# Kernel optimization log

Measured on AMD Instinct MI355X. Metric: run time of the kernel, lower is better.

## Reference

```python
import jax, jax.numpy as jnp
import numpy as np

B, S, D, H, L, E, FF = 16, 1024, 384, 8, 3, 8, 768
DH = D // H
TOP_K = 2


def _ln(x, s, b):
    m = x.mean(-1, keepdims=True)
    v = x.var(-1, keepdims=True)
    return (x - m) * jax.lax.rsqrt(v + 1e-5) * s + b


def setup_inputs() -> dict:
    key = jax.random.key(0)
    ks = jax.random.split(key, 12)
    def n(k, shp, scale=0.02):
        return jax.random.normal(k, shp, jnp.float32) * scale
    return dict(
        x=jax.random.normal(ks[0], (B, S, 1), jnp.float32),
        proj_w=n(ks[1], (1, D)), proj_b=jnp.zeros((D,), jnp.float32),
        qkv_w=n(ks[2], (L, D, 3 * D)), qkv_b=jnp.zeros((L, 3 * D), jnp.float32),
        out_w=n(ks[3], (L, D, D)), out_b=jnp.zeros((L, D), jnp.float32),
        n1_s=jnp.ones((L, D), jnp.float32), n1_b=jnp.zeros((L, D), jnp.float32),
        n2_s=jnp.ones((L, D), jnp.float32), n2_b=jnp.zeros((L, D), jnp.float32),
        gate_w=n(ks[4], (L, D, E)),
        e_w1=n(ks[5], (L, E, D, FF)), e_b1=jnp.zeros((L, E, FF), jnp.float32),
        e_w2=n(ks[6], (L, E, FF, D)), e_b2=jnp.zeros((L, E, D), jnp.float32),
        att_w=n(ks[7], (D,)), att_b=jnp.zeros((), jnp.float32),
        head_w=n(ks[8], (D, 1)), head_b=jnp.zeros((1,), jnp.float32),
    )


def reference(x, proj_w, proj_b, qkv_w, qkv_b, out_w, out_b,
              n1_s, n1_b, n2_s, n2_b, gate_w, e_w1, e_b1, e_w2, e_b2,
              att_w, att_b, head_w, head_b):
    # feature projection: [B,S,1] -> [B,S,D]
    h = x @ proj_w + proj_b
    total_moe = jnp.zeros((), h.dtype)
    scale = np.float32(1.0 / np.sqrt(DH))
    for l in range(L):
        # --- pre-norm multi-head self-attention ---
        xn = _ln(h, n1_s[l], n1_b[l])
        qkv = xn @ qkv_w[l] + qkv_b[l]
        q, k, v = jnp.split(qkv, 3, axis=-1)
        q = q.reshape(B, S, H, DH)
        k = k.reshape(B, S, H, DH)
        v = v.reshape(B, S, H, DH)
        attn = jax.nn.softmax(jnp.einsum('bqhd,bkhd->bhqk', q, k) * scale, axis=-1)
        ao = jnp.einsum('bhqk,bkhd->bqhd', attn, v).reshape(B, S, D)
        h = h + (ao @ out_w[l] + out_b[l])
        # --- pre-norm top-2 gated MoE FFN ---
        xn2 = _ln(h, n2_s[l], n2_b[l])
        probs = jax.nn.softmax(xn2 @ gate_w[l], axis=-1)            # [B,S,E]
        topv, topi = jax.lax.top_k(probs, TOP_K)
        gates = topv / topv.sum(-1, keepdims=True)                  # renormalized top-2
        full = (jax.nn.one_hot(topi, E, dtype=h.dtype) * gates[..., None]).sum(-2)  # [B,S,E]
        moe_out = jnp.zeros_like(h)
        for e in range(E):  # fixed small expert loop
            ye = jax.nn.relu(xn2 @ e_w1[l, e] + e_b1[l, e]) @ e_w2[l, e] + e_b2[l, e]
            moe_out = moe_out + full[..., e:e + 1] * ye
        h = h + moe_out
        # switch-style load-balancing aux loss
        importance = probs.reshape(-1, E).mean(0)
        load = (full > 0).astype(h.dtype).reshape(-1, E).mean(0)
        total_moe = total_moe + E * jnp.sum(importance * load)
    w = jax.nn.softmax(h @ att_w + att_b, axis=1)                   # [B,S]
    pooled = jnp.einsum('bs,bsd->bd', w, h)
    rul = pooled @ head_w + head_b                                  # [B,1]
    return rul, total_moe
```

## Files before the change

kernel.cpp:

```cpp
#include <hip/hip_runtime.h>
#include <hip/hip_bf16.h>
#include <math.h>

#define TOKENS 16384
#define DMODEL 384
#define SEQ 1024
#define NHEAD 8
#define DHEAD 48
#define NEXP 8
#define FFDIM 768
#define NL 3

typedef __bf16 bf16x8 __attribute__((ext_vector_type(8)));
typedef __bf16 bf16x4 __attribute__((ext_vector_type(4)));
typedef float f32x4 __attribute__((ext_vector_type(4)));

__global__ void init_kernel(float* total_moe) { *total_moe = 0.f; }

__global__ void zero_cnt_kernel(int* counts, float* sum_probs) {
  int t = threadIdx.x;
  if (t < NEXP) { counts[t] = 0; sum_probs[t] = 0.f; }
}

__global__ void finalize_kernel(const float* total_moe, float* out) { out[16] = *total_moe; }

__global__ __launch_bounds__(256) void proj_kernel(const float* __restrict__ x,
    const float* __restrict__ pw, const float* __restrict__ pb, float* __restrict__ h) {
  int i = blockIdx.x * 256 + threadIdx.x;
  int t = i / DMODEL;
  int d = i - t * DMODEL;
  h[i] = x[t] * pw[d] + pb[d];
}

__global__ __launch_bounds__(256) void convw_kernel(const float* __restrict__ src,
    __bf16* __restrict__ dst, int K, int N) {
  __shared__ float t[32][33];
  size_t boff = (size_t)blockIdx.z * K * N;
  src += boff; dst += boff;
  int k0 = blockIdx.y * 32, n0 = blockIdx.x * 32;
  int tx = threadIdx.x & 31, ty = threadIdx.x >> 5;
#pragma unroll
  for (int i = 0; i < 32; i += 8) t[ty + i][tx] = src[(size_t)(k0 + ty + i) * N + n0 + tx];
  __syncthreads();
#pragma unroll
  for (int i = 0; i < 32; i += 8)
    dst[(size_t)(n0 + ty + i) * K + k0 + tx] = (__bf16)t[tx][ty + i];
}

__global__ __launch_bounds__(384) void ln_kernel(const float* __restrict__ src,
    __bf16* __restrict__ dst, const float* __restrict__ gs, const float* __restrict__ gb) {
  int row = blockIdx.x, tid = threadIdx.x;
  float v = src[(size_t)row * DMODEL + tid];
  float sum = v, sq = v * v;
#pragma unroll
  for (int off = 32; off; off >>= 1) { sum += __shfl_xor(sum, off); sq += __shfl_xor(sq, off); }
  __shared__ float rs[6], rq[6];
  __shared__ float smean, sinv;
  int wid = tid >> 6;
  if ((tid & 63) == 0) { rs[wid] = sum; rq[wid] = sq; }
  __syncthreads();
  if (tid == 0) {
    float S = 0.f, Q = 0.f;
    for (int w = 0; w < 6; w++) { S += rs[w]; Q += rq[w]; }
    float mean = S / (float)DMODEL;
    float var = Q / (float)DMODEL - mean * mean;
    smean = mean; sinv = rsqrtf(var + 1e-5f);
  }
  __syncthreads();
  dst[(size_t)row * DMODEL + tid] = (__bf16)((v - smean) * sinv * gs[tid] + gb[tid]);
}

template<int MODE>
__global__ __launch_bounds__(256) void mgemm_kernel(
    const __bf16* __restrict__ Abf, const __bf16* __restrict__ Wt,
    const float* __restrict__ bias, float* __restrict__ Cf, __bf16* __restrict__ Cb,
    __bf16* __restrict__ pQ, __bf16* __restrict__ pK, __bf16* __restrict__ pV,
    const int* __restrict__ counts, const int* __restrict__ offs,
    const int* __restrict__ tok_list, const float* __restrict__ gate_list,
    int N, int K) {
  int e = 0, cnt = 0, base = 0;
  const int* tl = nullptr;
  int m0 = blockIdx.y * 128;
  int n0 = blockIdx.x * 128;
  if constexpr (MODE == 2 || MODE == 3) {
    e = blockIdx.z;
    cnt = counts[e];
    if (m0 >= cnt) return;
    base = offs[e];
    tl = tok_list + e * TOKENS;
    Wt += (size_t)e * N * K;
    bias += (size_t)e * N;
  }
  __shared__ __align__(16) __bf16 As[2][128][72];
  __shared__ __align__(16) __bf16 Bs[2][128][72];
  int tid = threadIdx.x;
  int w = tid >> 6, lane = tid & 63, c = lane & 15, g = lane >> 4;
  int arow[4], acol[4], brow[4], bcol4[4];
  long tok[4];
#pragma unroll
  for (int i = 0; i < 4; i++) {
    int chunk = tid + 256 * i;
    arow[i] = chunk >> 3;
    acol[i] = (chunk & 7) * 8;
    brow[i] = chunk >> 3;
    bcol4[i] = (chunk & 7) * 8;
    int mr = m0 + arow[i];
    if constexpr (MODE == 2)      tok[i] = (mr < cnt) ? (long)(tl[mr] & 0xFFFF) : -1;
    else if constexpr (MODE == 3) tok[i] = (mr < cnt) ? (long)(base + mr) : -1;
    else                          tok[i] = mr;
  }
  f32x4 acc[2][8];
#pragma unroll
  for (int m = 0; m < 2; m++)
#pragma unroll
    for (int n = 0; n < 8; n++) { acc[m][n][0] = 0.f; acc[m][n][1] = 0.f; acc[m][n][2] = 0.f; acc[m][n][3] = 0.f; }

  bf16x8 ra[4], rb[4];
  int nk = K >> 6;
#pragma unroll
  for (int i = 0; i < 4; i++) {
    bf16x8 v = {};
    if (tok[i] >= 0) v = *(const bf16x8*)&Abf[(size_t)tok[i] * K + acol[i]];
    ra[i] = v;
    rb[i] = *(const bf16x8*)&Wt[(size_t)(n0 + brow[i]) * K + bcol4[i]];
  }
  for (int kt = 0; kt < nk; kt++) {
    int cb = kt & 1;
#pragma unroll
    for (int i = 0; i < 4; i++) {
      *(bf16x8*)&As[cb][arow[i]][acol[i]] = ra[i];
      *(bf16x8*)&Bs[cb][brow[i]][bcol4[i]] = rb[i];
    }
    __syncthreads();
    if (kt + 1 < nk) {
      int k0 = (kt + 1) << 6;
#pragma unroll
      for (int i = 0; i < 4; i++) {
        bf16x8 v = {};
        if (tok[i] >= 0) v = *(const bf16x8*)&Abf[(size_t)tok[i] * K + k0 + acol[i]];
        ra[i] = v;
        rb[i] = *(const bf16x8*)&Wt[(size_t)(n0 + brow[i]) * K + k0 + bcol4[i]];
      }
    }
#pragma unroll
    for (int kk = 0; kk < 2; kk++) {
      bf16x8 a0 = *(const bf16x8*)&As[cb][w * 32 + c][kk * 32 + g * 8];
      bf16x8 a1 = *(const bf16x8*)&As[cb][w * 32 + 16 + c][kk * 32 + g * 8];
#pragma unroll
      for (int n = 0; n < 8; n++) {
        bf16x8 b = *(const bf16x8*)&Bs[cb][n * 16 + c][kk * 32 + g * 8];
        acc[0][n] = __builtin_amdgcn_mfma_f32_16x16x32_bf16(a0, b, acc[0][n], 0, 0, 0);
        acc[1][n] = __builtin_amdgcn_mfma_f32_16x16x32_bf16(a1, b, acc[1][n], 0, 0, 0);
      }
    }
  }
#pragma unroll
  for (int m = 0; m < 2; m++) {
    int row = w * 32 + m * 16 + 4 * g;
#pragma unroll
    for (int n = 0; n < 8; n++) {
      int col = n0 + n * 16 + c;
      float bv = bias[col];
#pragma unroll
      for (int r = 0; r < 4; r++) {
        float v = acc[m][n][r] + bv;
        int lr = row + r;
        if constexpr (MODE == 0) {
          int t = m0 + lr;
          int b = t >> 10, s = t & 1023;
          int which = col / 384;
          int rem = col - which * 384;
          int hd = rem / 48;
          int d = rem - hd * 48;
          size_t bh = (size_t)(b * 8 + hd);
          if (which == 0)      pQ[(bh * 1024 + s) * 48 + d] = (__bf16)(v * 0.14433756729740643f);
          else if (which == 1) pK[(bh * 1024 + s) * 48 + d] = (__bf16)v;
          else                 pV[(bh * 48 + d) * 1024 + s] = (__bf16)v;
        } else if constexpr (MODE == 1) {
          Cf[(size_t)(m0 + lr) * N + col] += v;
        } else if constexpr (MODE == 2) {
          if (m0 + lr < cnt) Cb[(size_t)(base + m0 + lr) * N + col] = (__bf16)fmaxf(v, 0.f);
        } else {
          if (m0 + lr < cnt) {
            int entry = tl[m0 + lr];
            int t = entry & 0xFFFF, a = entry >> 16;
            float gv = gate_list[e * TOKENS + m0 + lr];
            Cb[((size_t)a * TOKENS + t) * DMODEL + col] = (__bf16)(gv * v);
          }
        }
      }
    }
  }
}

__global__ __launch_bounds__(256) void combine_kernel(float* __restrict__ h,
    const __bf16* __restrict__ ab) {
  size_t i = ((size_t)blockIdx.x * 256 + threadIdx.x) * 8;
  bf16x8 a0 = *(const bf16x8*)&ab[i];
  bf16x8 a1 = *(const bf16x8*)&ab[(size_t)TOKENS * DMODEL + i];
  float* hp = h + i;
#pragma unroll
  for (int j = 0; j < 8; j++) hp[j] += (float)a0[j] + (float)a1[j];
}

__global__ __launch_bounds__(256) void attn_kernel(const __bf16* __restrict__ Qh,
    const __bf16* __restrict__ Kh, const __bf16* __restrict__ VTh,
    __bf16* __restrict__ ao) {
  __shared__ __align__(16) __bf16 Ks[64][56];
  __shared__ __align__(16) __bf16 Vt[48][72];
  __shared__ __align__(16) __bf16 Ps[4][16][72];
  int bh = blockIdx.x;
  int q0 = blockIdx.y * 64;
  int tid = threadIdx.x;
  int w = tid >> 6, lane = tid & 63, c = lane & 15, g = lane >> 4;

  const __bf16* qrow = Qh + ((size_t)bh * 1024 + q0 + w * 16 + c) * 48;
  bf16x8 qb0 = *(const bf16x8*)&qrow[g * 8];
  bf16x8 qb1 = {};
  if (g < 2) qb1 = *(const bf16x8*)&qrow[32 + g * 8];

  const __bf16* kb = Kh + (size_t)bh * 1024 * 48;
  const __bf16* vb = VTh + (size_t)bh * 48 * 1024;

  int r0 = tid / 6, p0 = tid - r0 * 6;
  __bf16* dst0 = &Ks[r0][p0 * 8];
  int off0 = r0 * 48 + p0 * 8;
  int e1 = tid + 256;
  __bf16* dst1; int off1; bool v1;
  if (e1 < 384) { int r = e1 / 6, p = e1 - r * 6; dst1 = &Ks[r][p * 8]; off1 = r * 48 + p * 8; v1 = false; }
  else          { int i = e1 - 384; int d = i >> 3, p = i & 7; dst1 = &Vt[d][p * 8]; off1 = d * 1024 + p * 8; v1 = true; }
  int i2 = tid + 512 - 384;
  int d2 = i2 >> 3, p2 = i2 & 7;
  __bf16* dst2 = &Vt[d2][p2 * 8];
  int off2 = d2 * 1024 + p2 * 8;

  f32x4 acc[3];
#pragma unroll
  for (int t = 0; t < 3; t++) { acc[t][0] = 0.f; acc[t][1] = 0.f; acc[t][2] = 0.f; acc[t][3] = 0.f; }
  float lsum = 0.f;

  for (int kt = 0; kt < 16; kt++) {
    __syncthreads();
    const __bf16* kbt = kb + (size_t)kt * 3072;
    const __bf16* vbt = vb + kt * 64;
    *(bf16x8*)dst0 = *(const bf16x8*)(kbt + off0);
    *(bf16x8*)dst1 = *(const bf16x8*)((v1 ? vbt : kbt) + off1);
    *(bf16x8*)dst2 = *(const bf16x8*)(vbt + off2);
    __syncthreads();

    f32x4 s4[4];
#pragma unroll
    for (int f = 0; f < 4; f++) {
      bf16x8 ka0 = *(const bf16x8*)&Ks[f * 16 + c][g * 8];
      bf16x8 ka1 = {};
      if (g < 2) ka1 = *(const bf16x8*)&Ks[f * 16 + c][32 + g * 8];
      f32x4 z = {};
      z = __builtin_amdgcn_mfma_f32_16x16x32_bf16(ka0, qb0, z, 0, 0, 0);
      s4[f] = __builtin_amdgcn_mfma_f32_16x16x32_bf16(ka1, qb1, z, 0, 0, 0);
    }
#pragma unroll
    for (int f = 0; f < 4; f++) {
      float pv0 = __expf(s4[f][0]);
      float pv1 = __expf(s4[f][1]);
      float pv2 = __expf(s4[f][2]);
      float pv3 = __expf(s4[f][3]);
      lsum += (pv0 + pv1) + (pv2 + pv3);
      bf16x4 pk = { (__bf16)pv0, (__bf16)pv1, (__bf16)pv2, (__bf16)pv3 };
      *(bf16x4*)&Ps[w][c][f * 16 + 4 * g] = pk;
    }
    bf16x8 pa0 = *(const bf16x8*)&Ps[w][c][g * 8];
    bf16x8 pa1 = *(const bf16x8*)&Ps[w][c][32 + g * 8];
#pragma unroll
    for (int t = 0; t < 3; t++) {
      bf16x8 vb0 = *(const bf16x8*)&Vt[t * 16 + c][g * 8];
      bf16x8 vb1 = *(const bf16x8*)&Vt[t * 16 + c][32 + g * 8];
      acc[t] = __builtin_amdgcn_mfma_f32_16x16x32_bf16(pa0, vb0, acc[t], 0, 0, 0);
      acc[t] = __builtin_amdgcn_mfma_f32_16x16x32_bf16(pa1, vb1, acc[t], 0, 0, 0);
    }
  }
  float lt = lsum;
  lt += __shfl_xor(lt, 16, 64);
  lt += __shfl_xor(lt, 32, 64);
  float linv[4];
#pragma unroll
  for (int r = 0; r < 4; r++) linv[r] = 1.f / __shfl(lt, 4 * g + r, 64);
  int b = bh >> 3, hh = bh & 7;
#pragma unroll
  for (int t = 0; t < 3; t++)
#pragma unroll
    for (int r = 0; r < 4; r++)
      ao[((size_t)(b * SEQ + q0 + w * 16 + 4 * g + r)) * DMODEL + hh * 48 + t * 16 + c] =
          (__bf16)(acc[t][r] * linv[r]);
}

__global__ __launch_bounds__(256) void gate_kernel(const __bf16* __restrict__ xnb,
    const float* __restrict__ gw, int* __restrict__ counts, float* __restrict__ sum_probs,
    int* __restrict__ tok_list, float* __restrict__ gate_list) {
  __shared__ float Gs[NEXP][DMODEL];
  __shared__ float simp[NEXP];
  __shared__ int hist[NEXP], basep[NEXP];
  __shared__ unsigned char tokE[32][2];
  __shared__ float tokG[32][2];
  __shared__ short rankS[32][2];
  int tid = threadIdx.x;
  for (int i = tid; i < DMODEL * NEXP; i += 256) {
    int d = i >> 3, e2 = i & 7;
    Gs[e2][d] = gw[i];
  }
  if (tid < NEXP) { simp[tid] = 0.f; hist[tid] = 0; }
  __syncthreads();
  int w = tid >> 6, lane = tid & 63;
  int tbase = blockIdx.x * 32 + w * 8;
  float impacc[NEXP] = {};
  for (int tt = 0; tt < 8; tt++) {
    int t = tbase + tt;
    float p[NEXP] = {};
#pragma unroll
    for (int j = 0; j < 6; j++) {
      int d = lane + 64 * j;
      float xv = (float)xnb[(size_t)t * DMODEL + d];
#pragma unroll
      for (int e2 = 0; e2 < NEXP; e2++) p[e2] += xv * Gs[e2][d];
    }
#pragma unroll
    for (int off = 32; off; off >>= 1)
#pragma unroll
      for (int e2 = 0; e2 < NEXP; e2++) p[e2] += __shfl_xor(p[e2], off);
    float mx = p[0];
#pragma unroll
    for (int e2 = 1; e2 < NEXP; e2++) mx = fmaxf(mx, p[e2]);
    float s = 0.f;
#pragma unroll
    for (int e2 = 0; e2 < NEXP; e2++) { p[e2] = __expf(p[e2] - mx); s += p[e2]; }
    float inv = 1.f / s;
#pragma unroll
    for (int e2 = 0; e2 < NEXP; e2++) { p[e2] *= inv; impacc[e2] += p[e2]; }
    int i0 = 0; float v0 = p[0];
#pragma unroll
    for (int e2 = 1; e2 < NEXP; e2++) if (p[e2] > v0) { v0 = p[e2]; i0 = e2; }
    int i1 = -1; float v1 = -INFINITY;
#pragma unroll
    for (int e2 = 0; e2 < NEXP; e2++) if (e2 != i0 && p[e2] > v1) { v1 = p[e2]; i1 = e2; }
    if (lane == 0) {
      float gsum = v0 + v1;
      int r0 = atomicAdd(&hist[i0], 1);
      int r1 = atomicAdd(&hist[i1], 1);
      int sl = w * 8 + tt;
      tokE[sl][0] = (unsigned char)i0; tokE[sl][1] = (unsigned char)i1;
      tokG[sl][0] = v0 / gsum;         tokG[sl][1] = v1 / gsum;
      rankS[sl][0] = (short)r0;        rankS[sl][1] = (short)r1;
    }
  }
  if (lane == 0)
#pragma unroll
    for (int e2 = 0; e2 < NEXP; e2++) atomicAdd(&simp[e2], impacc[e2]);
  __syncthreads();
  if (tid < NEXP) {
    basep[tid] = atomicAdd(&counts[tid], hist[tid]);
    atomicAdd(&sum_probs[tid], simp[tid]);
  }
  __syncthreads();
  int t0 = blockIdx.x * 32;
  if (tid < 64) {
    int sl = tid >> 1, a = tid & 1;
    int e2 = tokE[sl][a];
    int pos = basep[e2] + rankS[sl][a];
    tok_list[e2 * TOKENS + pos] = (t0 + sl) | (a << 16);
    gate_list[e2 * TOKENS + pos] = tokG[sl][a];
  }
}

__global__ void aux_kernel(const int* __restrict__ counts, int* __restrict__ offs,
                           const float* __restrict__ sum_probs, float* __restrict__ total_moe) {
  int off = 0;
  float tm = 0.f;
  for (int e = 0; e < NEXP; e++) {
    offs[e] = off;
    off += ((counts[e] + 63) >> 6) << 6;
    tm += sum_probs[e] * (float)counts[e];
  }
  offs[NEXP] = off;
  *total_moe += (float)NEXP * tm / ((float)TOKENS * (float)TOKENS);
}

__global__ __launch_bounds__(256) void head1_kernel(const float* __restrict__ h,
    const float* __restrict__ att_w, const float* __restrict__ att_b,
    float* __restrict__ logits) {
  int tid = threadIdx.x;
  int w = tid >> 6, lane = tid & 63;
  float4 aw0 = *(const float4*)&att_w[lane * 4];
  float2 aw1 = *(const float2*)&att_w[256 + lane * 2];
  float ab = att_b[0];
  for (int i = w; i < 32; i += 4) {
    int t = blockIdx.x * 32 + i;
    const float* hr = h + (size_t)t * DMODEL;
    float4 v4 = *(const float4*)&hr[lane * 4];
    float2 v2 = *(const float2*)&hr[256 + lane * 2];
    float dot = v4.x * aw0.x + v4.y * aw0.y + v4.z * aw0.z + v4.w * aw0.w
              + v2.x * aw1.x + v2.y * aw1.y;
#pragma unroll
    for (int off = 32; off; off >>= 1) dot += __shfl_xor(dot, off);
    if (lane == 0) logits[t] = dot + ab;
  }
}

__global__ __launch_bounds__(256) void head2_kernel(float* __restrict__ logits) {
  int b = blockIdx.x, tid = threadIdx.x;
  int w = tid >> 6, lane = tid & 63;
  float* lb = logits + b * SEQ;
  __shared__ float red[4];
  float lv[4];
  float mx = -INFINITY;
#pragma unroll
  for (int i = 0; i < 4; i++) { lv[i] = lb[tid + 256 * i]; mx = fmaxf(mx, lv[i]); }
#pragma unroll
  for (int off = 32; off; off >>= 1) mx = fmaxf(mx, __shfl_xor(mx, off));
  if (lane == 0) red[w] = mx;
  __syncthreads();
  mx = fmaxf(fmaxf(red[0], red[1]), fmaxf(red[2], red[3]));
  __syncthreads();
  float s = 0.f;
#pragma unroll
  for (int i = 0; i < 4; i++) { lv[i] = __expf(lv[i] - mx); s += lv[i]; }
#pragma unroll
  for (int off = 32; off; off >>= 1) s += __shfl_xor(s, off);
  if (lane == 0) red[w] = s;
  __syncthreads();
  float inv = 1.f / (red[0] + red[1] + red[2] + red[3]);
#pragma unroll
  for (int i = 0; i < 4; i++) lb[tid + 256 * i] = lv[i] * inv;
}

__global__ __launch_bounds__(256) void head3a_kernel(const float* __restrict__ h,
    const float* __restrict__ wnorm, float* __restrict__ partial) {
  int b = blockIdx.x, dc = blockIdx.y, sc = blockIdx.z;
  int tid = threadIdx.x;
  int d = tid & 63, sg = tid >> 6;
  const float* hb = h + (size_t)b * SEQ * DMODEL + dc * 64 + d;
  const float* wb = wnorm + b * SEQ + sc * 64;
  float acc = 0.f;
  int s0 = sc * 64 + sg * 16;
#pragma unroll
  for (int i = 0; i < 16; i++)
    acc += wb[sg * 16 + i] * hb[(size_t)(s0 + i) * DMODEL];
  __shared__ float red[256];
  red[tid] = acc;
  __syncthreads();
  if (sg == 0)
    partial[(((size_t)b * 6 + dc) * 16 + sc) * 64 + d] =
        red[d] + red[64 + d] + red[128 + d] + red[192 + d];
}

__global__ void head3b_kernel(const float* __restrict__ partial,
    const float* __restrict__ head_w, float* __restrict__ part) {
  int b = blockIdx.x, dc = blockIdx.y;
  int d = threadIdx.x;
  const float* pp = partial + (((size_t)b * 6 + dc) * 16) * 64 + d;
  float pooled = 0.f;
#pragma unroll
  for (int sc = 0; sc < 16; sc++) pooled += pp[sc * 64];
  float pd = pooled * head_w[dc * 64 + d];
#pragma unroll
  for (int off = 32; off; off >>= 1) pd += __shfl_xor(pd, off);
  if (d == 0) part[b * 6 + dc] = pd;
}

__global__ void head4_kernel(const float* __restrict__ part,
                             const float* __restrict__ head_b, float* __restrict__ out) {
  int b = threadIdx.x;
  if (b < 16) {
    float s = head_b[0];
#pragma unroll
    for (int dc = 0; dc < 6; dc++) s += part[b * 6 + dc];
    out[b] = s;
  }
}

extern "C" void kernel_launch(void* const* d_in, const int* in_sizes, int n_in,
                              void* d_out, int out_size, void* d_ws, size_t ws_size,
                              hipStream_t stream) {
  (void)in_sizes; (void)n_in; (void)out_size; (void)ws_size;
  const float* x      = (const float*)d_in[0];
  const float* proj_w = (const float*)d_in[1];
  const float* proj_b = (const float*)d_in[2];
  const float* qkv_w  = (const float*)d_in[3];
  const float* qkv_b  = (const float*)d_in[4];
  const float* out_w  = (const float*)d_in[5];
  const float* out_b  = (const float*)d_in[6];
  const float* n1_s   = (const float*)d_in[7];
  const float* n1_b   = (const float*)d_in[8];
  const float* n2_s   = (const float*)d_in[9];
  const float* n2_b   = (const float*)d_in[10];
  const float* gate_w = (const float*)d_in[11];
  const float* e_w1   = (const float*)d_in[12];
  const float* e_b1   = (const float*)d_in[13];
  const float* e_w2   = (const float*)d_in[14];
  const float* e_b2   = (const float*)d_in[15];
  const float* att_w  = (const float*)d_in[16];
  const float* att_b  = (const float*)d_in[17];
  const float* head_w = (const float*)d_in[18];
  const float* head_b = (const float*)d_in[19];
  float* out = (float*)d_out;

  char* wsb = (char*)d_ws;
  float*  h    = (float*)(wsb);
  __bf16* xnb  = (__bf16*)(wsb + 25165824);
  __bf16* aob  = (__bf16*)(wsb + 37748736);
  __bf16* ab   = (__bf16*)(wsb + 25165824);
  __bf16* uni  = (__bf16*)(wsb + 50331648);
  __bf16* Qh   = uni;
  __bf16* Khd  = (__bf16*)(wsb + 62914560);
  __bf16* VTh  = (__bf16*)(wsb + 75497472);
  __bf16* qkvWt = (__bf16*)(wsb + 101449728);
  __bf16* outWt = (__bf16*)(wsb + 104103936);
  __bf16* e1Wt  = (__bf16*)(wsb + 104988672);
  __bf16* e2Wt  = (__bf16*)(wsb + 119144448);
  char* sm = wsb + 133300224;
  int*   counts    = (int*)(sm);
  int*   offs      = (int*)(sm + 64);
  float* sum_probs = (float*)(sm + 128);
  float* total_moe = (float*)(sm + 192);
  int*   tok_list  = (int*)(sm + 256);
  float* gate_list = (float*)(sm + 256 + 524288);
  float* logits    = (float*)(sm + 1048832);
  float* part      = (float*)(sm + 1048832 + 65536);
  float* partial   = (float*)(sm + 1048832 + 131072);

  convw_kernel<<<dim3(36, 12, 3), 256, 0, stream>>>(qkv_w, qkvWt, 384, 1152);
  convw_kernel<<<dim3(12, 12, 3), 256, 0, stream>>>(out_w, outWt, 384, 384);
  convw_kernel<<<dim3(24, 12, 24), 256, 0, stream>>>(e_w1, e1Wt, 384, 768);
  convw_kernel<<<dim3(12, 24, 24), 256, 0, stream>>>(e_w2, e2Wt, 768, 384);

  init_kernel<<<1, 1, 0, stream>>>(total_moe);
  proj_kernel<<<TOKENS * DMODEL / 256, 256, 0, stream>>>(x, proj_w, proj_b, h);

  for (int l = 0; l < NL; l++) {
    ln_kernel<<<TOKENS, 384, 0, stream>>>(h, xnb, n1_s + l * DMODEL, n1_b + l * DMODEL);
    mgemm_kernel<0><<<dim3(9, 128), 256, 0, stream>>>(
        xnb, qkvWt + (size_t)l * 1152 * 384, qkv_b + l * 1152, nullptr, nullptr,
        Qh, Khd, VTh, nullptr, nullptr, nullptr, nullptr, 1152, 384);
    attn_kernel<<<dim3(128, 16), 256, 0, stream>>>(Qh, Khd, VTh, aob);
    mgemm_kernel<1><<<dim3(3, 128), 256, 0, stream>>>(
        aob, outWt + (size_t)l * 384 * 384, out_b + l * 384, h, nullptr,
        nullptr, nullptr, nullptr, nullptr, nullptr, nullptr, nullptr, 384, 384);
    ln_kernel<<<TOKENS, 384, 0, stream>>>(h, xnb, n2_s + l * DMODEL, n2_b + l * DMODEL);
    zero_cnt_kernel<<<1, 64, 0, stream>>>(counts, sum_probs);
    gate_kernel<<<512, 256, 0, stream>>>(xnb, gate_w + (size_t)l * DMODEL * NEXP,
                                         counts, sum_probs, tok_list, gate_list);
    aux_kernel<<<1, 1, 0, stream>>>(counts, offs, sum_probs, total_moe);
    mgemm_kernel<2><<<dim3(6, 128, 8), 256, 0, stream>>>(
        xnb, e1Wt + (size_t)l * 8 * 768 * 384, e_b1 + l * 8 * FFDIM, nullptr, uni,
        nullptr, nullptr, nullptr, counts, offs, tok_list, nullptr, 768, 384);
    mgemm_kernel<3><<<dim3(3, 128, 8), 256, 0, stream>>>(
        uni, e2Wt + (size_t)l * 8 * 384 * 768, e_b2 + l * 8 * DMODEL, nullptr, ab,
        nullptr, nullptr, nullptr, counts, offs, tok_list, gate_list, 384, 768);
    combine_kernel<<<TOKENS * DMODEL / (256 * 8), 256, 0, stream>>>(h, ab);
  }

  head1_kernel<<<512, 256, 0, stream>>>(h, att_w, att_b, logits);
  head2_kernel<<<16, 256, 0, stream>>>(logits);
  head3a_kernel<<<dim3(16, 6, 16), 256, 0, stream>>>(h, logits, partial);
  head3b_kernel<<<dim3(16, 6), 64, 0, stream>>>(partial, head_w, part);
  head4_kernel<<<1, 64, 0, stream>>>(part, head_b, out);
  finalize_kernel<<<1, 1, 0, stream>>>(total_moe, out);
}
```

Before: 1.073 ms.

## Fuse MoE expert up and down projections into one kernel per token tile

```diff
diff --git a/kernel.cpp b/kernel.cpp
--- a/kernel.cpp
+++ b/kernel.cpp
@@ -73,41 +73,21 @@
 template<int MODE>
 __global__ __launch_bounds__(256) void mgemm_kernel(
     const __bf16* __restrict__ Abf, const __bf16* __restrict__ Wt,
-    const float* __restrict__ bias, float* __restrict__ Cf, __bf16* __restrict__ Cb,
+    const float* __restrict__ bias, float* __restrict__ Cf,
     __bf16* __restrict__ pQ, __bf16* __restrict__ pK, __bf16* __restrict__ pV,
-    const int* __restrict__ counts, const int* __restrict__ offs,
-    const int* __restrict__ tok_list, const float* __restrict__ gate_list,
     int N, int K) {
-  int e = 0, cnt = 0, base = 0;
-  const int* tl = nullptr;
   int m0 = blockIdx.y * 128;
   int n0 = blockIdx.x * 128;
-  if constexpr (MODE == 2 || MODE == 3) {
-    e = blockIdx.z;
-    cnt = counts[e];
-    if (m0 >= cnt) return;
-    base = offs[e];
-    tl = tok_list + e * TOKENS;
-    Wt += (size_t)e * N * K;
-    bias += (size_t)e * N;
-  }
   __shared__ __align__(16) __bf16 As[2][128][72];
   __shared__ __align__(16) __bf16 Bs[2][128][72];
   int tid = threadIdx.x;
   int w = tid >> 6, lane = tid & 63, c = lane & 15, g = lane >> 4;
-  int arow[4], acol[4], brow[4], bcol4[4];
-  long tok[4];
+  int arow[4], acol[4];
 #pragma unroll
   for (int i = 0; i < 4; i++) {
     int chunk = tid + 256 * i;
     arow[i] = chunk >> 3;
     acol[i] = (chunk & 7) * 8;
-    brow[i] = chunk >> 3;
-    bcol4[i] = (chunk & 7) * 8;
-    int mr = m0 + arow[i];
-    if constexpr (MODE == 2)      tok[i] = (mr < cnt) ? (long)(tl[mr] & 0xFFFF) : -1;
-    else if constexpr (MODE == 3) tok[i] = (mr < cnt) ? (long)(base + mr) : -1;
-    else                          tok[i] = mr;
   }
   f32x4 acc[2][8];
 #pragma unroll
@@ -119,27 +99,23 @@
   int nk = K >> 6;
 #pragma unroll
   for (int i = 0; i < 4; i++) {
-    bf16x8 v = {};
-    if (tok[i] >= 0) v = *(const bf16x8*)&Abf[(size_t)tok[i] * K + acol[i]];
-    ra[i] = v;
-    rb[i] = *(const bf16x8*)&Wt[(size_t)(n0 + brow[i]) * K + bcol4[i]];
+    ra[i] = *(const bf16x8*)&Abf[(size_t)(m0 + arow[i]) * K + acol[i]];
+    rb[i] = *(const bf16x8*)&Wt[(size_t)(n0 + arow[i]) * K + acol[i]];
   }
   for (int kt = 0; kt < nk; kt++) {
     int cb = kt & 1;
 #pragma unroll
     for (int i = 0; i < 4; i++) {
       *(bf16x8*)&As[cb][arow[i]][acol[i]] = ra[i];
-      *(bf16x8*)&Bs[cb][brow[i]][bcol4[i]] = rb[i];
+      *(bf16x8*)&Bs[cb][arow[i]][acol[i]] = rb[i];
     }
     __syncthreads();
     if (kt + 1 < nk) {
       int k0 = (kt + 1) << 6;
 #pragma unroll
       for (int i = 0; i < 4; i++) {
-        bf16x8 v = {};
-        if (tok[i] >= 0) v = *(const bf16x8*)&Abf[(size_t)tok[i] * K + k0 + acol[i]];
-        ra[i] = v;
-        rb[i] = *(const bf16x8*)&Wt[(size_t)(n0 + brow[i]) * K + k0 + bcol4[i]];
+        ra[i] = *(const bf16x8*)&Abf[(size_t)(m0 + arow[i]) * K + k0 + acol[i]];
+        rb[i] = *(const bf16x8*)&Wt[(size_t)(n0 + arow[i]) * K + k0 + acol[i]];
       }
     }
 #pragma unroll
@@ -176,21 +152,114 @@
           if (which == 0)      pQ[(bh * 1024 + s) * 48 + d] = (__bf16)(v * 0.14433756729740643f);
           else if (which == 1) pK[(bh * 1024 + s) * 48 + d] = (__bf16)v;
           else                 pV[(bh * 48 + d) * 1024 + s] = (__bf16)v;
-        } else if constexpr (MODE == 1) {
+        } else {
           Cf[(size_t)(m0 + lr) * N + col] += v;
-        } else if constexpr (MODE == 2) {
-          if (m0 + lr < cnt) Cb[(size_t)(base + m0 + lr) * N + col] = (__bf16)fmaxf(v, 0.f);
-        } else {
-          if (m0 + lr < cnt) {
-            int entry = tl[m0 + lr];
-            int t = entry & 0xFFFF, a = entry >> 16;
-            float gv = gate_list[e * TOKENS + m0 + lr];
-            Cb[((size_t)a * TOKENS + t) * DMODEL + col] = (__bf16)(gv * v);
-          }
         }
       }
     }
   }
+}
+
+__global__ __launch_bounds__(256) void moe_fused_kernel(
+    const __bf16* __restrict__ xnb, const __bf16* __restrict__ W1t,
+    const __bf16* __restrict__ W2t, const float* __restrict__ b1,
+    const float* __restrict__ b2, __bf16* __restrict__ ab,
+    const int* __restrict__ counts, const int* __restrict__ tok_list,
+    const float* __restrict__ gate_list) {
+  int e = blockIdx.y;
+  int cnt = counts[e];
+  int m0 = blockIdx.x * 32;
+  if (m0 >= cnt) return;
+  const int* tl = tok_list + e * TOKENS;
+  const float* gl = gate_list + e * TOKENS;
+  W1t += (size_t)e * FFDIM * DMODEL;
+  W2t += (size_t)e * DMODEL * FFDIM;
+  b1 += e * FFDIM;
+  b2 += e * DMODEL;
+  __shared__ __align__(16) __bf16 Xs[32][392];
+  __shared__ __align__(16) __bf16 A1s[32][776];
+  int tid = threadIdx.x;
+  int w = tid >> 6, lane = tid & 63, c = lane & 15, g = lane >> 4;
+  {
+    int row = tid >> 3, part = tid & 7;
+    int mr = m0 + row;
+    int tok = tl[mr < cnt ? mr : cnt - 1] & 0xFFFF;
+    const __bf16* src = xnb + (size_t)tok * DMODEL + part * 48;
+#pragma unroll
+    for (int i = 0; i < 6; i++)
+      *(bf16x8*)&Xs[row][part * 48 + i * 8] = *(const bf16x8*)&src[i * 8];
+  }
+  __syncthreads();
+  for (int ni = 0; ni < 3; ni++) {
+    int nb = w * 192 + ni * 64;
+    f32x4 acc[2][4];
+#pragma unroll
+    for (int mf = 0; mf < 2; mf++)
+#pragma unroll
+      for (int nf = 0; nf < 4; nf++) { acc[mf][nf][0] = 0.f; acc[mf][nf][1] = 0.f; acc[mf][nf][2] = 0.f; acc[mf][nf][3] = 0.f; }
+#pragma unroll
+    for (int kf = 0; kf < 12; kf++) {
+      bf16x8 a0 = *(const bf16x8*)&Xs[c][kf * 32 + g * 8];
+      bf16x8 a1 = *(const bf16x8*)&Xs[16 + c][kf * 32 + g * 8];
+#pragma unroll
+      for (int nf = 0; nf < 4; nf++) {
+        bf16x8 b = *(const bf16x8*)&W1t[(size_t)(nb + nf * 16 + c) * DMODEL + kf * 32 + g * 8];
+        acc[0][nf] = __builtin_amdgcn_mfma_f32_16x16x32_bf16(a0, b, acc[0][nf], 0, 0, 0);
+        acc[1][nf] = __builtin_amdgcn_mfma_f32_16x16x32_bf16(a1, b, acc[1][nf], 0, 0, 0);
+      }
+    }
+#pragma unroll
+    for (int mf = 0; mf < 2; mf++)
+#pragma unroll
+      for (int nf = 0; nf < 4; nf++) {
+        int col = nb + nf * 16 + c;
+        float bv = b1[col];
+#pragma unroll
+        for (int r = 0; r < 4; r++)
+          A1s[mf * 16 + 4 * g + r][col] = (__bf16)fmaxf(acc[mf][nf][r] + bv, 0.f);
+      }
+  }
+  __syncthreads();
+  f32x4 acc2[2][6];
+#pragma unroll
+  for (int mf = 0; mf < 2; mf++)
+#pragma unroll
+    for (int nf = 0; nf < 6; nf++) { acc2[mf][nf][0] = 0.f; acc2[mf][nf][1] = 0.f; acc2[mf][nf][2] = 0.f; acc2[mf][nf][3] = 0.f; }
+  for (int kf = 0; kf < 24; kf++) {
+    bf16x8 a0 = *(const bf16x8*)&A1s[c][kf * 32 + g * 8];
+    bf16x8 a1 = *(const bf16x8*)&A1s[16 + c][kf * 32 + g * 8];
+#pragma unroll
+    for (int nf = 0; nf < 6; nf++) {
+      bf16x8 b = *(const bf16x8*)&W2t[(size_t)(w * 96 + nf * 16 + c) * FFDIM + kf * 32 + g * 8];
+      acc2[0][nf] = __builtin_amdgcn_mfma_f32_16x16x32_bf16(a0, b, acc2[0][nf], 0, 0, 0);
+      acc2[1][nf] = __builtin_amdgcn_mfma_f32_16x16x32_bf16(a1, b, acc2[1][nf], 0, 0, 0);
+    }
+  }
+  int rowt[2][4];
+  float rowg[2][4];
+#pragma unroll
+  for (int mf = 0; mf < 2; mf++)
+#pragma unroll
+    for (int r = 0; r < 4; r++) {
+      int row = m0 + mf * 16 + 4 * g + r;
+      if (row < cnt) { rowt[mf][r] = tl[row]; rowg[mf][r] = gl[row]; }
+      else rowt[mf][r] = -1;
+    }
+#pragma unroll
+  for (int mf = 0; mf < 2; mf++)
+#pragma unroll
+    for (int nf = 0; nf < 6; nf++) {
+      int col = w * 96 + nf * 16 + c;
+      float bv = b2[col];
+#pragma unroll
+      for (int r = 0; r < 4; r++) {
+        int entry = rowt[mf][r];
+        if (entry >= 0) {
+          int t = entry & 0xFFFF, a = entry >> 16;
+          ab[((size_t)a * TOKENS + t) * DMODEL + col] = (__bf16)(rowg[mf][r] * (acc2[mf][nf][r] + bv));
+        }
+      }
+    }
 }
 
 __global__ __launch_bounds__(256) void combine_kernel(float* __restrict__ h,
@@ -370,16 +439,10 @@
   }
 }
 
-__global__ void aux_kernel(const int* __restrict__ counts, int* __restrict__ offs,
+__global__ void aux_kernel(const int* __restrict__ counts,
                            const float* __restrict__ sum_probs, float* __restrict__ total_moe) {
-  int off = 0;
   float tm = 0.f;
-  for (int e = 0; e < NEXP; e++) {
-    offs[e] = off;
-    off += ((counts[e] + 63) >> 6) << 6;
-    tm += sum_probs[e] * (float)counts[e];
-  }
-  offs[NEXP] = off;
+  for (int e = 0; e < NEXP; e++) tm += sum_probs[e] * (float)counts[e];
   *total_moe += (float)NEXP * tm / ((float)TOKENS * (float)TOKENS);
 }
 
@@ -507,8 +570,7 @@
   __bf16* xnb  = (__bf16*)(wsb + 25165824);
   __bf16* aob  = (__bf16*)(wsb + 37748736);
   __bf16* ab   = (__bf16*)(wsb + 25165824);
-  __bf16* uni  = (__bf16*)(wsb + 50331648);
-  __bf16* Qh   = uni;
+  __bf16* Qh   = (__bf16*)(wsb + 50331648);
   __bf16* Khd  = (__bf16*)(wsb + 62914560);
   __bf16* VTh  = (__bf16*)(wsb + 75497472);
   __bf16* qkvWt = (__bf16*)(wsb + 101449728);
@@ -517,7 +579,6 @@
   __bf16* e2Wt  = (__bf16*)(wsb + 119144448);
   char* sm = wsb + 133300224;
   int*   counts    = (int*)(sm);
-  int*   offs      = (int*)(sm + 64);
   float* sum_probs = (float*)(sm + 128);
   float* total_moe = (float*)(sm + 192);
   int*   tok_list  = (int*)(sm + 256);
@@ -537,23 +598,21 @@
   for (int l = 0; l < NL; l++) {
     ln_kernel<<<TOKENS, 384, 0, stream>>>(h, xnb, n1_s + l * DMODEL, n1_b + l * DMODEL);
     mgemm_kernel<0><<<dim3(9, 128), 256, 0, stream>>>(
-        xnb, qkvWt + (size_t)l * 1152 * 384, qkv_b + l * 1152, nullptr, nullptr,
-        Qh, Khd, VTh, nullptr, nullptr, nullptr, nullptr, 1152, 384);
+        xnb, qkvWt + (size_t)l * 1152 * 384, qkv_b + l * 1152, nullptr,
+        Qh, Khd, VTh, 1152, 384);
     attn_kernel<<<dim3(128, 16), 256, 0, stream>>>(Qh, Khd, VTh, aob);
     mgemm_kernel<1><<<dim3(3, 128), 256, 0, stream>>>(
-        aob, outWt + (size_t)l * 384 * 384, out_b + l * 384, h, nullptr,
-        nullptr, nullptr, nullptr, nullptr, nullptr, nullptr, nullptr, 384, 384);
+        aob, outWt + (size_t)l * 384 * 384, out_b + l * 384, h,
+        nullptr, nullptr, nullptr, 384, 384);
     ln_kernel<<<TOKENS, 384, 0, stream>>>(h, xnb, n2_s + l * DMODEL, n2_b + l * DMODEL);
     zero_cnt_kernel<<<1, 64, 0, stream>>>(counts, sum_probs);
     gate_kernel<<<512, 256, 0, stream>>>(xnb, gate_w + (size_t)l * DMODEL * NEXP,
                                          counts, sum_probs, tok_list, gate_list);
-    aux_kernel<<<1, 1, 0, stream>>>(counts, offs, sum_probs, total_moe);
-    mgemm_kernel<2><<<dim3(6, 128, 8), 256, 0, stream>>>(
-        xnb, e1Wt + (size_t)l * 8 * 768 * 384, e_b1 + l * 8 * FFDIM, nullptr, uni,
-        nullptr, nullptr, nullptr, counts, offs, tok_list, nullptr, 768, 384);
-    mgemm_kernel<3><<<dim3(3, 128, 8), 256, 0, stream>>>(
-        uni, e2Wt + (size_t)l * 8 * 384 * 768, e_b2 + l * 8 * DMODEL, nullptr, ab,
-        nullptr, nullptr, nullptr, counts, offs, tok_list, gate_list, 384, 768);
+    aux_kernel<<<1, 1, 0, stream>>>(counts, sum_probs, total_moe);
+    moe_fused_kernel<<<dim3(512, 8), 256, 0, stream>>>(
+        xnb, e1Wt + (size_t)l * 8 * 768 * 384, e2Wt + (size_t)l * 8 * 384 * 768,
+        e_b1 + l * 8 * FFDIM, e_b2 + l * 8 * DMODEL, ab,
+        counts, tok_list, gate_list);
     combine_kernel<<<TOKENS * DMODEL / (256 * 8), 256, 0, stream>>>(h, ab);
   }
 
```

Result: slower. 1.347 ms (+25.5%).
